# Optimization experiments

Measured on AMD Instinct MI355X. Metric: run time of the kernel, lower is better.

## Reference

```python
import jax, jax.numpy as jnp
import numpy as np
import math

B, N, D = 16, 1024, 1024

def setup_inputs() -> dict:
    key = jax.random.key(0)
    k1, k2, k3, k4 = jax.random.split(key, 4)
    x = jax.random.normal(k1, (B, N, D), dtype=jnp.float32)
    # Keras 'random_normal' initializer defaults to stddev=0.05
    w_keys = jax.random.normal(k2, (N, N), dtype=jnp.float32) * 0.05
    w_queries = jax.random.normal(k3, (N, N), dtype=jnp.float32) * 0.05
    w_values = jax.random.normal(k4, (N, N), dtype=jnp.float32) * 0.05
    return {"x": x, "w_keys": w_keys, "w_queries": w_queries, "w_values": w_values}

def reference(x, w_keys, w_queries, w_values):
    # x: (B, N, D); weights: (N, N); fact = sqrt(N) per build(input_shape[1])
    fact = math.sqrt(x.shape[1])
    ip = jnp.swapaxes(x, 1, 2)              # (B, D, N)
    vk = ip @ w_keys                         # (B, D, N)
    vq = ip @ w_queries                      # (B, D, N)
    vv = ip @ w_values                       # (B, D, N)
    kq = jnp.einsum('bdn,ben->bde', vk, vq) / fact   # (B, D, D)
    sm = jax.nn.softmax(kq, axis=-1)         # softmax over last axis
    # tf: sm @ transpose(pm(vv)) == sm @ vv  since pm then transpose_b cancel
    out = jnp.einsum('bde,ben->bdn', sm, vv) # (B, D, N)
    return jnp.swapaxes(out, 1, 2)           # (B, N, D)
```

## Files before the change

### kernel.cpp

```cpp
#include <hip/hip_runtime.h>
#include <stdint.h>


typedef __bf16 bf16x8_t __attribute__((ext_vector_type(8)));
typedef float  f32x4_t  __attribute__((ext_vector_type(4)));

typedef __attribute__((address_space(3))) uint32_t as3_u32;
typedef __attribute__((address_space(1))) uint32_t as1_u32;

__device__ __forceinline__ void async_copy16(const void* g, const void* l) {
  __builtin_amdgcn_global_load_lds((const as1_u32*)(uintptr_t)g,
                                   (as3_u32*)(uint32_t)(uintptr_t)l,
                                   16, 0, 0);
}

__device__ __forceinline__ uint16_t f2bf(float f) {
  uint32_t x = __float_as_uint(f);
  return (uint16_t)((x + 0x7fffu + ((x >> 16) & 1u)) >> 16);
}
__device__ __forceinline__ float bf2f(uint16_t b) {
  return __uint_as_float(((uint32_t)b) << 16);
}

template <int EPI>
__global__ __launch_bounds__(512, 4)
void gemm_bt256x128(const uint16_t* __restrict__ A,
                    const uint16_t* __restrict__ B,
                    void* __restrict__ Cv, size_t sA, size_t sB, size_t sC,
                    float alpha, float* __restrict__ Sp)
{
  __shared__ __align__(16) char smem[49152];
  char* As = smem;
  char* Bs = smem + 32768;

  const int lid  = blockIdx.x;
  const int xcd  = lid & 7;
  const int slot = lid >> 3;
  const int z    = (xcd << 1) | (slot >> 5);
  const int t32  = slot & 31;
  const int bm0  = (t32 >> 3) << 8;
  const int bn0  = (t32 & 7) << 7;

  A += (size_t)z * sA + ((size_t)bm0 << 10);
  B += (size_t)z * sB + ((size_t)bn0 << 10);

  const int t    = threadIdx.x;
  const int lane = t & 63;
  const int w    = t >> 6;
  const int q    = lane >> 4;
  const int r16  = lane & 15;
  const int wm   = (w >> 1) << 6;
  const int wn   = (w & 1) << 6;

  const int g0  = t >> 3;
  const int cp  = t & 7;
  const int ce  = (cp ^ (g0 & 7)) << 3;
  const int so  = (g0 << 7) + (cp << 4);
  const uint16_t* Ag = A + ((size_t)g0 << 10) + ce;
  const uint16_t* Bg = B + ((size_t)g0 << 10) + ce;

  f32x4_t acc[4][4];
#pragma unroll
  for (int i = 0; i < 4; i++)
#pragma unroll
    for (int j = 0; j < 4; j++) acc[i][j] = (f32x4_t){0.f, 0.f, 0.f, 0.f};

  for (int k0 = 0; k0 < 1024; k0 += 64) {
#pragma unroll
    for (int s = 0; s < 4; ++s)
      async_copy16(Ag + (((size_t)s << 6) << 10) + k0, As + so + (s << 13));
#pragma unroll
    for (int s = 0; s < 2; ++s)
      async_copy16(Bg + (((size_t)s << 6) << 10) + k0, Bs + so + (s << 13));
    __syncthreads();

#pragma unroll
    for (int kk = 0; kk < 2; ++kk) {
      bf16x8_t af[4], bfr[4];
#pragma unroll
      for (int mi = 0; mi < 4; ++mi) {
        const int m = wm + (mi << 4) + r16;
        const int c = (kk << 2) + q;
        af[mi] = *(const bf16x8_t*)(As + (m << 7) + ((c ^ (m & 7)) << 4));
      }
#pragma unroll
      for (int ni = 0; ni < 4; ++ni) {
        const int n = wn + (ni << 4) + r16;
        const int c = (kk << 2) + q;
        bfr[ni] = *(const bf16x8_t*)(Bs + (n << 7) + ((c ^ (n & 7)) << 4));
      }
      __builtin_amdgcn_s_setprio(1);
#pragma unroll
      for (int mi = 0; mi < 4; ++mi)
#pragma unroll
        for (int ni = 0; ni < 4; ++ni)
          acc[mi][ni] = __builtin_amdgcn_mfma_f32_16x16x32_bf16(
              af[mi], bfr[ni], acc[mi][ni], 0, 0, 0);
      __builtin_amdgcn_s_setprio(0);
    }
    __syncthreads();
  }

  if constexpr (EPI == 3) {
    float inv[4];
#pragma unroll
    for (int ni = 0; ni < 4; ++ni) {
      const int c = bn0 + wn + (ni << 4) + r16;
      float S = 0.f;
#pragma unroll
      for (int p = 0; p < 16; ++p)
        S += Sp[((size_t)p << 14) + ((size_t)z << 10) + c];
      inv[ni] = 1.0f / S;
    }
    float* C = (float*)Cv + (size_t)z * sC;
#pragma unroll
    for (int mi = 0; mi < 4; ++mi)
#pragma unroll
      for (int ni = 0; ni < 4; ++ni)
#pragma unroll
        for (int r = 0; r < 4; ++r) {
          const int row = bm0 + wm + (mi << 4) + (q << 2) + r;
          const int col = bn0 + wn + (ni << 4) + r16;
          C[((size_t)row << 10) + col] = acc[mi][ni][r] * alpha * inv[ni];
        }
  } else {
    float* reg = (float*)smem + (size_t)w * 1056;
    uint16_t* C = (uint16_t*)Cv + (size_t)z * sC;
    float* SpW = Sp + ((size_t)(((bn0 >> 7) << 1) + (w & 1)) << 14)
                    + ((size_t)z << 10);
#pragma unroll
    for (int mi = 0; mi < 4; ++mi) {
      if constexpr (EPI == 2) {
        float ev[4][4];
#pragma unroll
        for (int ni = 0; ni < 4; ++ni)
#pragma unroll
          for (int r = 0; r < 4; ++r) {
            ev[ni][r] = __expf(acc[mi][ni][r] * alpha);
            reg[((q << 2) + r) * 66 + (ni << 4) + r16] = ev[ni][r];
          }
#pragma unroll
        for (int r = 0; r < 4; ++r) {
          float s = ev[0][r] + ev[1][r] + ev[2][r] + ev[3][r];
          s += __shfl_xor(s, 1, 16);
          s += __shfl_xor(s, 2, 16);
          s += __shfl_xor(s, 4, 16);
          s += __shfl_xor(s, 8, 16);
          if (r16 == 0)
            SpW[bm0 + wm + (mi << 4) + (q << 2) + r] = s;
        }
      } else {
#pragma unroll
        for (int ni = 0; ni < 4; ++ni)
#pragma unroll
          for (int r = 0; r < 4; ++r)
            reg[((q << 2) + r) * 66 + (ni << 4) + r16] = acc[mi][ni][r] * alpha;
      }
#pragma unroll
      for (int it = 0; it < 8; ++it) {
        const int rr = (it << 1) + (lane >> 5);
        const int cc = (lane & 31) << 1;
        const float2 v = *(const float2*)(reg + rr * 66 + cc);
        const uint32_t p = (uint32_t)f2bf(v.x) | ((uint32_t)f2bf(v.y) << 16);
        const int row = bm0 + wm + (mi << 4) + rr;
        const int col = bn0 + wn + cc;
        *(uint32_t*)(C + ((size_t)row << 10) + col) = p;
      }
    }
  }
}

__global__ __launch_bounds__(256, 4)
void gemm128_splitk(const uint16_t* __restrict__ A, const uint16_t* __restrict__ B,
                    float* __restrict__ P)
{
  __shared__ __align__(16) char smem[32768];
  char* As = smem;
  char* Bs = smem + 16384;

  const int slice = blockIdx.x >> 6;
  const int tile  = blockIdx.x & 63;
  const int bm0   = (tile >> 3) << 7;
  const int bn0   = (tile & 7) << 7;
  const int koff  = slice << 8;

  const int t    = threadIdx.x;
  const int lane = t & 63;
  const int w    = t >> 6;
  const int q    = lane >> 4;
  const int r16  = lane & 15;
  const int wm   = (w >> 1) << 6;
  const int wn   = (w & 1) << 6;

  f32x4_t acc[4][4];
#pragma unroll
  for (int i = 0; i < 4; i++)
#pragma unroll
    for (int j = 0; j < 4; j++) acc[i][j] = (f32x4_t){0.f, 0.f, 0.f, 0.f};

  for (int k0 = koff; k0 < koff + 256; k0 += 64) {
#pragma unroll
    for (int i = 0; i < 4; i++) {
      const int o  = (i << 12) + (t << 4);
      const int m  = o >> 7;
      const int cp = (o >> 4) & 7;
      const int c  = cp ^ (m & 7);
      async_copy16(A + (size_t)(bm0 + m) * 1024 + (size_t)(k0 + (c << 3)), As + o);
      async_copy16(B + (size_t)(bn0 + m) * 1024 + (size_t)(k0 + (c << 3)), Bs + o);
    }
    __syncthreads();
#pragma unroll
    for (int kk = 0; kk < 2; kk++) {
      bf16x8_t af[4], bfr[4];
#pragma unroll
      for (int mi = 0; mi < 4; mi++) {
        const int m = wm + (mi << 4) + r16;
        const int c = (kk << 2) + q;
        af[mi] = *(const bf16x8_t*)(As + (m << 7) + ((c ^ (m & 7)) << 4));
      }
#pragma unroll
      for (int ni = 0; ni < 4; ni++) {
        const int n = wn + (ni << 4) + r16;
        const int c = (kk << 2) + q;
        bfr[ni] = *(const bf16x8_t*)(Bs + (n << 7) + ((c ^ (n & 7)) << 4));
      }
#pragma unroll
      for (int mi = 0; mi < 4; mi++)
#pragma unroll
        for (int ni = 0; ni < 4; ni++)
          acc[mi][ni] = __builtin_amdgcn_mfma_f32_16x16x32_bf16(
              af[mi], bfr[ni], acc[mi][ni], 0, 0, 0);
    }
    __syncthreads();
  }

  float* C = P + (size_t)slice * (1024u * 1024u);
#pragma unroll
  for (int mi = 0; mi < 4; mi++)
#pragma unroll
    for (int ni = 0; ni < 4; ni++)
#pragma unroll
      for (int r = 0; r < 4; r++) {
        const int row = bm0 + wm + (mi << 4) + (q << 2) + r;
        const int col = bn0 + wn + (ni << 4) + r16;
        C[((size_t)row << 10) + col] = acc[mi][ni][r];
      }
}

__global__ __launch_bounds__(256)
void reduce_w2t(const float* __restrict__ P, uint16_t* __restrict__ W)
{
  const size_t i4 = (((size_t)blockIdx.x << 8) + threadIdx.x) << 2;
  const float4 a = *(const float4*)(P + i4);
  const float4 b = *(const float4*)(P + (1u << 20) + i4);
  const float4 c = *(const float4*)(P + (2u << 20) + i4);
  const float4 d = *(const float4*)(P + (3u << 20) + i4);
  ushort4 r;
  r.x = f2bf(a.x + b.x + c.x + d.x);
  r.y = f2bf(a.y + b.y + c.y + d.y);
  r.z = f2bf(a.z + b.z + c.z + d.z);
  r.w = f2bf(a.w + b.w + c.w + d.w);
  *(ushort4*)(W + i4) = r;
}

__global__ __launch_bounds__(256)
void prep_w(const float* __restrict__ w0, const float* __restrict__ w1,
            const float* __restrict__ w2, uint16_t* __restrict__ o0,
            uint16_t* __restrict__ o1, uint16_t* __restrict__ o2)
{
  __shared__ float tile[32][33];
  const int z = blockIdx.z;
  const int c0 = blockIdx.x << 5;
  const int r0 = blockIdx.y << 5;
  const int tx = threadIdx.x;
  const int ty = threadIdx.y;
  if (z < 2) {
    const float* src = z ? w1 : w0;
    uint16_t* dst = z ? o1 : o0;
#pragma unroll
    for (int i = 0; i < 32; i += 8)
      dst[(size_t)(r0 + ty + i) * 1024 + (c0 + tx)] =
          f2bf(src[(size_t)(r0 + ty + i) * 1024 + (c0 + tx)]);
  } else {
#pragma unroll
    for (int i = 0; i < 32; i += 8)
      tile[ty + i][tx] = w2[(size_t)(r0 + ty + i) * 1024 + (c0 + tx)];
    __syncthreads();
#pragma unroll
    for (int i = 0; i < 32; i += 8)
      o2[(size_t)(c0 + ty + i) * 1024 + (r0 + tx)] = f2bf(tile[tx][ty + i]);
  }
}

__global__ __launch_bounds__(256)
void transpose_cast(const float* __restrict__ src, uint16_t* __restrict__ dst,
                    int R, int Ccols, size_t sStride, size_t dStride)
{
  __shared__ float tile[32][33];
  const int z = blockIdx.z;
  src += (size_t)z * sStride;
  dst += (size_t)z * dStride;
  const int c0 = blockIdx.x << 5;
  const int r0 = blockIdx.y << 5;
  const int tx = threadIdx.x;
  const int ty = threadIdx.y;
#pragma unroll
  for (int i = 0; i < 32; i += 8)
    tile[ty + i][tx] = src[(size_t)(r0 + ty + i) * Ccols + (c0 + tx)];
  __syncthreads();
#pragma unroll
  for (int i = 0; i < 32; i += 8)
    dst[(size_t)(c0 + ty + i) * R + (r0 + tx)] = f2bf(tile[tx][ty + i]);
}

extern "C" void kernel_launch(void* const* d_in, const int* in_sizes, int n_in,
                              void* d_out, int out_size, void* d_ws, size_t ws_size,
                              hipStream_t stream)
{
  const float* x  = (const float*)d_in[0];
  const float* wk = (const float*)d_in[1];
  const float* wq = (const float*)d_in[2];
  const float* wv = (const float*)d_in[3];
  float* out = (float*)d_out;

  constexpr int BB = 16, N = 1024, D = 1024;
  constexpr size_t DN = (size_t)D * N;

  char* ws = (char*)d_ws;
  uint16_t* xT   = (uint16_t*)(ws);
  uint16_t* Wkc  = (uint16_t*)(ws + (32ull << 20));
  uint16_t* Wqc  = (uint16_t*)(ws + (34ull << 20));
  uint16_t* Wtv  = (uint16_t*)(ws + (36ull << 20));
  uint16_t* W2Tc = (uint16_t*)(ws + (38ull << 20));
  float*    W2p  = (float*)   (ws + (40ull << 20));
  uint16_t* tmp  = (uint16_t*)(ws + (56ull << 20));
  uint16_t* vvT  = (uint16_t*)(ws + (88ull << 20));
  uint16_t* P    = (uint16_t*)(ws + (120ull << 20));
  float*    Spart= (float*)   (ws + (152ull << 20));

  const dim3 tb(32, 8);
  prep_w<<<dim3(N / 32, N / 32, 3), tb, 0, stream>>>(wk, wq, wv, Wkc, Wqc, Wtv);
  gemm128_splitk<<<256, 256, 0, stream>>>(Wqc, Wkc, W2p);
  reduce_w2t<<<1024, 256, 0, stream>>>(W2p, W2Tc);
  transpose_cast<<<dim3(D / 32, N / 32, BB), tb, 0, stream>>>(x, xT, N, D, DN, DN);
  gemm_bt256x128<0><<<512, 512, 0, stream>>>(xT, W2Tc, tmp, DN, 0, DN, 1.0f, Spart);
  gemm_bt256x128<0><<<512, 512, 0, stream>>>(Wtv, xT, vvT, 0, DN, DN, 1.0f, Spart);
  gemm_bt256x128<2><<<512, 512, 0, stream>>>(tmp, xT, P, DN, DN, DN, 0.03125f, Spart);
  gemm_bt256x128<3><<<512, 512, 0, stream>>>(vvT, P, out, DN, DN, DN, 1.0f, Spart);
}
```

Baseline: 282.5 us.

## Switch batched GEMMs to double-buffered 128x128 tiles with 256-thread blocks

Replaces the 256x128-tile, 512-thread GEMM with a 128x128-tile, 256-thread kernel. The new kernel keeps two LDS stages and prefetches the next K-slice with async global-to-LDS copies while the current slice is multiplied, so only one barrier is needed per iteration. The grid doubles to 1024 blocks. The aim is to hide global-load latency behind MFMA work and improve occupancy and load balance. In exchange it uses 64KB of LDS per block, which may cap resident blocks per CU, and each smaller tile gets less operand reuse.

```diff
diff --git a/kernel.cpp b/kernel.cpp
--- a/kernel.cpp
+++ b/kernel.cpp
@@ -23,23 +23,20 @@
 }
 
 template <int EPI>
-__global__ __launch_bounds__(512, 4)
-void gemm_bt256x128(const uint16_t* __restrict__ A,
-                    const uint16_t* __restrict__ B,
-                    void* __restrict__ Cv, size_t sA, size_t sB, size_t sC,
-                    float alpha, float* __restrict__ Sp)
-{
-  __shared__ __align__(16) char smem[49152];
-  char* As = smem;
-  char* Bs = smem + 32768;
+__global__ __launch_bounds__(256, 4)
+void gemm_bt128d(const uint16_t* __restrict__ A, const uint16_t* __restrict__ B,
+                 void* __restrict__ Cv, size_t sA, size_t sB, size_t sC,
+                 float alpha, float* __restrict__ Sp)
+{
+  __shared__ __align__(16) char smem[65536];
 
   const int lid  = blockIdx.x;
   const int xcd  = lid & 7;
   const int slot = lid >> 3;
-  const int z    = (xcd << 1) | (slot >> 5);
-  const int t32  = slot & 31;
-  const int bm0  = (t32 >> 3) << 8;
-  const int bn0  = (t32 & 7) << 7;
+  const int z    = (xcd << 1) | (slot >> 6);
+  const int t64  = slot & 63;
+  const int bm0  = (t64 >> 3) << 7;
+  const int bn0  = (t64 & 7) << 7;
 
   A += (size_t)z * sA + ((size_t)bm0 << 10);
   B += (size_t)z * sB + ((size_t)bn0 << 10);
@@ -52,28 +49,33 @@
   const int wm   = (w >> 1) << 6;
   const int wn   = (w & 1) << 6;
 
-  const int g0  = t >> 3;
-  const int cp  = t & 7;
-  const int ce  = (cp ^ (g0 & 7)) << 3;
-  const int so  = (g0 << 7) + (cp << 4);
-  const uint16_t* Ag = A + ((size_t)g0 << 10) + ce;
-  const uint16_t* Bg = B + ((size_t)g0 << 10) + ce;
-
   f32x4_t acc[4][4];
 #pragma unroll
   for (int i = 0; i < 4; i++)
 #pragma unroll
     for (int j = 0; j < 4; j++) acc[i][j] = (f32x4_t){0.f, 0.f, 0.f, 0.f};
 
-  for (int k0 = 0; k0 < 1024; k0 += 64) {
-#pragma unroll
-    for (int s = 0; s < 4; ++s)
-      async_copy16(Ag + (((size_t)s << 6) << 10) + k0, As + so + (s << 13));
-#pragma unroll
-    for (int s = 0; s < 2; ++s)
-      async_copy16(Bg + (((size_t)s << 6) << 10) + k0, Bs + so + (s << 13));
-    __syncthreads();
-
+#define STAGE128(kk0, dbase) do {                                              \
+    _Pragma("unroll")                                                          \
+    for (int i = 0; i < 4; i++) {                                              \
+      const int o  = (i << 12) + (t << 4);                                     \
+      const int m  = o >> 7;                                                   \
+      const int cp = (o >> 4) & 7;                                             \
+      const int c  = cp ^ (m & 7);                                             \
+      async_copy16(A + ((size_t)m << 10) + (size_t)((kk0) + (c << 3)),         \
+                   smem + (dbase) + o);                                        \
+      async_copy16(B + ((size_t)m << 10) + (size_t)((kk0) + (c << 3)),         \
+                   smem + (dbase) + 16384 + o);                                \
+    } } while (0)
+
+  STAGE128(0, 0);
+  __syncthreads();
+
+  int cur = 0;
+  for (int t0 = 0; t0 < 16; ++t0) {
+    if (t0 < 15) STAGE128((t0 + 1) << 6, cur ^ 32768);
+    const char* As = smem + cur;
+    const char* Bs = smem + cur + 16384;
 #pragma unroll
     for (int kk = 0; kk < 2; ++kk) {
       bf16x8_t af[4], bfr[4];
@@ -99,7 +101,9 @@
       __builtin_amdgcn_s_setprio(0);
     }
     __syncthreads();
+    cur ^= 32768;
   }
+#undef STAGE128
 
   if constexpr (EPI == 3) {
     float inv[4];
@@ -343,8 +347,8 @@
   gemm128_splitk<<<256, 256, 0, stream>>>(Wqc, Wkc, W2p);
   reduce_w2t<<<1024, 256, 0, stream>>>(W2p, W2Tc);
   transpose_cast<<<dim3(D / 32, N / 32, BB), tb, 0, stream>>>(x, xT, N, D, DN, DN);
-  gemm_bt256x128<0><<<512, 512, 0, stream>>>(xT, W2Tc, tmp, DN, 0, DN, 1.0f, Spart);
-  gemm_bt256x128<0><<<512, 512, 0, stream>>>(Wtv, xT, vvT, 0, DN, DN, 1.0f, Spart);
-  gemm_bt256x128<2><<<512, 512, 0, stream>>>(tmp, xT, P, DN, DN, DN, 0.03125f, Spart);
-  gemm_bt256x128<3><<<512, 512, 0, stream>>>(vvT, P, out, DN, DN, DN, 1.0f, Spart);
-}
+  gemm_bt128d<0><<<1024, 256, 0, stream>>>(xT, W2Tc, tmp, DN, 0, DN, 1.0f, Spart);
+  gemm_bt128d<0><<<1024, 256, 0, stream>>>(Wtv, xT, vvT, 0, DN, DN, 1.0f, Spart);
+  gemm_bt128d<2><<<1024, 256, 0, stream>>>(tmp, xT, P, DN, DN, DN, 0.03125f, Spart);
+  gemm_bt128d<3><<<1024, 256, 0, stream>>>(vvT, P, out, DN, DN, DN, 1.0f, Spart);
+}
```

Result: slower. 301.9 us (+6.9%).
